# Kernel optimization log

Measured on AMD Instinct MI355X. Metric: run time of the kernel, lower is better.

## Reference

```python
import jax, jax.numpy as jnp
import numpy as np

B, H, W, C = 4, 64, 64, 64
DK = C // 8  # key/query channels from Conv2D(filters=channels//8)


def setup_inputs() -> dict:
    key = jax.random.key(0)
    ks = jax.random.split(key, 4)
    x = jax.random.normal(ks[0], (B, H, W, C), dtype=jnp.float32)
    # he_normal-ish scale for 1x1 conv kernels (fan_in = C)
    s = np.sqrt(2.0 / C).astype(np.float32)
    Wf = jax.random.normal(ks[1], (C, DK), dtype=jnp.float32) * s
    Wg = jax.random.normal(ks[2], (C, DK), dtype=jnp.float32) * s
    Wh = jax.random.normal(ks[3], (C, C), dtype=jnp.float32) * s
    bf = jnp.zeros((DK,), dtype=jnp.float32)
    bg = jnp.zeros((DK,), dtype=jnp.float32)
    bh = jnp.zeros((C,), dtype=jnp.float32)
    return {"x": x, "Wf": Wf, "bf": bf, "Wg": Wg, "bg": bg, "Wh": Wh, "bh": bh}


def reference(x, Wf, bf, Wg, bg, Wh, bh):
    b, h, w, c = x.shape
    n = h * w
    xf = x.reshape(b, n, c)  # 1x1 conv == per-position linear over flattened spatial dims
    f = xf @ Wf + bf         # [B, N, DK]
    g = xf @ Wg + bg         # [B, N, DK]
    v = xf @ Wh + bh         # [B, N, C]
    # attention = softmax(g @ f^T) over keys (tf.nn.softmax default: last axis)
    scores = jnp.einsum('bnd,bmd->bnm', g, f)   # [B, N, N]
    attn = jax.nn.softmax(scores, axis=-1)
    out = jnp.einsum('bnm,bmc->bnc', attn, v)   # [B, N, C]
    return out
```

## Files before the change

### kernel.cpp

```cpp
#include <hip/hip_runtime.h>
#include <hip/hip_bf16.h>
#include <hip/hip_fp16.h>

typedef _Float16 half8_t  __attribute__((ext_vector_type(8)));
typedef short    short8_t __attribute__((ext_vector_type(8)));
typedef short    short4_t __attribute__((ext_vector_type(4)));
typedef float    f32x4    __attribute__((ext_vector_type(4)));

#define LOG2E 1.44269504088896f

__device__ __forceinline__ unsigned pack_bf16_2(float lo, float hi) {
  float2 f2; f2.x = lo; f2.y = hi;
  __hip_bfloat162 h2 = __float22bfloat162_rn(f2);
  return *reinterpret_cast<unsigned*>(&h2);
}

__global__ __launch_bounds__(512) void prep_kernel(
    const float* __restrict__ x,
    const float* __restrict__ Wf, const float* __restrict__ bf,
    const float* __restrict__ Wg, const float* __restrict__ bg,
    const float* __restrict__ Wh, const float* __restrict__ bh,
    _Float16* __restrict__ fh, _Float16* __restrict__ gh,
    unsigned short* __restrict__ vT)
{
  __shared__ _Float16 WtT[80 * 72];
  __shared__ float ball[80];
  const int t = threadIdx.x;

  {
    int c = t >> 3, d = t & 7;
    WtT[d * 72 + c]       = (_Float16)Wf[t];
    WtT[(8 + d) * 72 + c] = (_Float16)(Wg[t] * LOG2E);
  }
#pragma unroll
  for (int rep = 0; rep < 2; rep++) {
    int i4 = t + rep * 512;
    float4 wv4 = *(const float4*)(Wh + i4 * 4);
    int c  = i4 >> 4;
    int ch = (i4 & 15) * 4;
    WtT[(16 + ch + 0) * 72 + c] = (_Float16)wv4.x;
    WtT[(16 + ch + 1) * 72 + c] = (_Float16)wv4.y;
    WtT[(16 + ch + 2) * 72 + c] = (_Float16)wv4.z;
    WtT[(16 + ch + 3) * 72 + c] = (_Float16)wv4.w;
  }
  if (t < 80) ball[t] = (t < 8) ? bf[t] : (t < 16) ? bg[t - 8] * LOG2E : bh[t - 16];
  __syncthreads();

  const int lane = t & 63, wv = t >> 6;
  const int quad = lane >> 4, l15 = lane & 15;
  const int wr   = wv & 3;
  const int hsel = wv >> 2;
  const int p0  = blockIdx.x * 64;
  const int row = p0 + wr * 16 + l15;

  const float* xr = x + (size_t)row * 64 + quad * 8;
  float4 xa = *(const float4*)(xr);
  float4 xb = *(const float4*)(xr + 4);
  float4 xc = *(const float4*)(xr + 32);
  float4 xd = *(const float4*)(xr + 36);
  half8_t a0, a1;
  a0[0]=(_Float16)xa.x; a0[1]=(_Float16)xa.y; a0[2]=(_Float16)xa.z; a0[3]=(_Float16)xa.w;
  a0[4]=(_Float16)xb.x; a0[5]=(_Float16)xb.y; a0[6]=(_Float16)xb.z; a0[7]=(_Float16)xb.w;
  a1[0]=(_Float16)xc.x; a1[1]=(_Float16)xc.y; a1[2]=(_Float16)xc.z; a1[3]=(_Float16)xc.w;
  a1[4]=(_Float16)xd.x; a1[5]=(_Float16)xd.y; a1[6]=(_Float16)xd.z; a1[7]=(_Float16)xd.w;

  const f32x4 zc = {0.f, 0.f, 0.f, 0.f};
  const int b     = p0 >> 12;
  const int nbase = (p0 & 4095) + wr * 16 + quad * 4;
  const int kblock = nbase >> 5;
  const int r0     = nbase & 31;
  const int q8 = r0 >> 3, j8 = r0 & 7;
  const int slot0 = (j8 < 4) ? (q8 * 4 + j8) : (16 + q8 * 4 + (j8 - 4));
  const size_t fbase_out = ((size_t)b * 4096 + (kblock << 5) + slot0) * 8;
  const size_t gbase_out = ((size_t)p0 + wr * 16 + quad * 4) * 8;
  const size_t vbase_out = (((size_t)b * 128 + kblock) << 11) + r0;

  if (hsel == 0) {
    {
      const _Float16* wt = &WtT[l15 * 72 + quad * 8];
      half8_t b0 = *(const half8_t*)(wt);
      half8_t b1 = *(const half8_t*)(wt + 32);
      f32x4 d = __builtin_amdgcn_mfma_f32_16x16x32_f16(a0, b0, zc, 0, 0, 0);
      d = __builtin_amdgcn_mfma_f32_16x16x32_f16(a1, b1, d, 0, 0, 0);
      const float bias = ball[l15];
      if (l15 < 8) {
#pragma unroll
        for (int reg = 0; reg < 4; reg++)
          fh[fbase_out + (size_t)reg * 8 + l15] = (_Float16)(d[reg] + bias);
      } else {
#pragma unroll
        for (int reg = 0; reg < 4; reg++)
          gh[gbase_out + (size_t)reg * 8 + (l15 - 8)] = (_Float16)(d[reg] + bias);
      }
    }
#pragma unroll
    for (int nt = 1; nt < 3; nt++) {
      const int ch0 = nt * 16 + l15;
      const _Float16* wt = &WtT[ch0 * 72 + quad * 8];
      half8_t b0 = *(const half8_t*)(wt);
      half8_t b1 = *(const half8_t*)(wt + 32);
      f32x4 d = __builtin_amdgcn_mfma_f32_16x16x32_f16(a0, b0, zc, 0, 0, 0);
      d = __builtin_amdgcn_mfma_f32_16x16x32_f16(a1, b1, d, 0, 0, 0);
      const float bias = ball[ch0];
      const int vch = ch0 - 16;
      union { unsigned u[2]; short4_t s; } pk;
      pk.u[0] = pack_bf16_2(d[0] + bias, d[1] + bias);
      pk.u[1] = pack_bf16_2(d[2] + bias, d[3] + bias);
      *(short4_t*)(vT + vbase_out + (size_t)vch * 32) = pk.s;
    }
  } else {
#pragma unroll
    for (int nt = 3; nt < 5; nt++) {
      const int ch0 = nt * 16 + l15;
      const _Float16* wt = &WtT[ch0 * 72 + quad * 8];
      half8_t b0 = *(const half8_t*)(wt);
      half8_t b1 = *(const half8_t*)(wt + 32);
      f32x4 d = __builtin_amdgcn_mfma_f32_16x16x32_f16(a0, b0, zc, 0, 0, 0);
      d = __builtin_amdgcn_mfma_f32_16x16x32_f16(a1, b1, d, 0, 0, 0);
      const float bias = ball[ch0];
      const int vch = ch0 - 16;
      union { unsigned u[2]; short4_t s; } pk;
      pk.u[0] = pack_bf16_2(d[0] + bias, d[1] + bias);
      pk.u[1] = pack_bf16_2(d[2] + bias, d[3] + bias);
      *(short4_t*)(vT + vbase_out + (size_t)vch * 32) = pk.s;
    }
  }
}

__device__ __forceinline__ void compute_chunk(
    const half8_t& f0, const half8_t& f1,
    const short8_t& v0, const short8_t& v1,
    const short8_t& v2, const short8_t& v3,
    const half8_t (&gfrag)[4], const short8_t& ones8,
    f32x4 (&acc)[4][4], f32x4 (&acc4)[4])
{
  const f32x4 zc = {0.f, 0.f, 0.f, 0.f};
  __builtin_amdgcn_s_setprio(1);
#pragma unroll
  for (int tt = 0; tt < 4; tt++) {
    f32x4 s0 = __builtin_amdgcn_mfma_f32_16x16x32_f16(f0, gfrag[tt], zc, 0, 0, 0);
    f32x4 s1 = __builtin_amdgcn_mfma_f32_16x16x32_f16(f1, gfrag[tt], zc, 0, 0, 0);
    float p00 = __builtin_amdgcn_exp2f(s0[0]), p01 = __builtin_amdgcn_exp2f(s0[1]);
    float p02 = __builtin_amdgcn_exp2f(s0[2]), p03 = __builtin_amdgcn_exp2f(s0[3]);
    float p10 = __builtin_amdgcn_exp2f(s1[0]), p11 = __builtin_amdgcn_exp2f(s1[1]);
    float p12 = __builtin_amdgcn_exp2f(s1[2]), p13 = __builtin_amdgcn_exp2f(s1[3]);
    union { unsigned u[4]; short8_t v; } pu;
    pu.u[0] = pack_bf16_2(p00, p01);
    pu.u[1] = pack_bf16_2(p02, p03);
    pu.u[2] = pack_bf16_2(p10, p11);
    pu.u[3] = pack_bf16_2(p12, p13);
    short8_t pfrag = pu.v;
    acc[tt][0] = __builtin_amdgcn_mfma_f32_16x16x32_bf16(v0, pfrag, acc[tt][0], 0, 0, 0);
    acc[tt][1] = __builtin_amdgcn_mfma_f32_16x16x32_bf16(v1, pfrag, acc[tt][1], 0, 0, 0);
    acc[tt][2] = __builtin_amdgcn_mfma_f32_16x16x32_bf16(v2, pfrag, acc[tt][2], 0, 0, 0);
    acc[tt][3] = __builtin_amdgcn_mfma_f32_16x16x32_bf16(v3, pfrag, acc[tt][3], 0, 0, 0);
    acc4[tt]   = __builtin_amdgcn_mfma_f32_16x16x32_bf16(ones8, pfrag, acc4[tt], 0, 0, 0);
  }
  __builtin_amdgcn_s_setprio(0);
}

__global__ __launch_bounds__(512, 2) void attn_kernel(
    const _Float16* __restrict__ fh,
    const _Float16* __restrict__ gh,
    const unsigned short* __restrict__ vT,
    float* __restrict__ out)
{
  const int N    = 4096;
  const int lane = threadIdx.x & 63;
  const int w    = threadIdx.x >> 6;
  const int quad = lane >> 4;
  const int l15  = lane & 15;

  __shared__ float red[7][64][17];

  const int xcd = blockIdx.x & 7;
  const int b   = xcd >> 1;
  const int qg  = ((blockIdx.x >> 3) << 1) + (xcd & 1);
  const int q0  = qg * 64;
  const int kbase = w * 512;
  const int rot = ((qg >> 1) & 15) + ((w >> 2) << 3);

  const _Float16* fbase = fh + (size_t)b * N * 8;
  const _Float16* gbase = gh + (size_t)b * N * 8;
  const short*    vbat  = (const short*)vT + (size_t)b * 262144 + (l15 << 5) + (quad << 3);

  half8_t gfrag[4] = {{}, {}, {}, {}};
  if (quad == 0) {
#pragma unroll
    for (int tt = 0; tt < 4; tt++)
      gfrag[tt] = *(const half8_t*)(gbase + (size_t)(q0 + tt * 16 + l15) * 8);
  }

  const f32x4 zc = {0.f, 0.f, 0.f, 0.f};
  f32x4 acc[4][4];
  f32x4 acc4[4];
#pragma unroll
  for (int tt = 0; tt < 4; tt++) {
    acc4[tt] = zc;
#pragma unroll
    for (int ct = 0; ct < 4; ct++) acc[tt][ct] = zc;
  }

  short8_t ones8;
#pragma unroll
  for (int i = 0; i < 8; i++) ones8[i] = (short)0x3F80;

#define KOFF(j) (kbase + ((((j) + rot) & 15) << 5))
#define LOADC(k, F0, F1, V0, V1, V2, V3)                                  \
  {                                                                       \
    const int kk = (k);                                                   \
    if (quad == 0) {                                                      \
      F0 = *(const half8_t*)(fbase + (size_t)(kk + l15) * 8);             \
      F1 = *(const half8_t*)(fbase + (size_t)(kk + 16 + l15) * 8);        \
    }                                                                     \
    const short* vk = vbat + ((size_t)(kk >> 5) << 11);                   \
    V0 = *(const short8_t*)(vk);                                          \
    V1 = *(const short8_t*)(vk + 512);                                    \
    V2 = *(const short8_t*)(vk + 1024);                                   \
    V3 = *(const short8_t*)(vk + 1536);                                   \
  }

  half8_t  fA0 = {}, fA1 = {}, fB0 = {}, fB1 = {};
  half8_t  fC0 = {}, fC1 = {}, fD0 = {}, fD1 = {};
  short8_t vA0, vA1, vA2, vA3, vB0, vB1, vB2, vB3;
  short8_t vC0, vC1, vC2, vC3, vD0, vD1, vD2, vD3;

  LOADC(KOFF(0), fA0, fA1, vA0, vA1, vA2, vA3);
  LOADC(KOFF(1), fB0, fB1, vB0, vB1, vB2, vB3);

#pragma unroll 1
  for (int cc = 0; cc < 16; cc += 4) {
    LOADC(KOFF(cc + 2), fC0, fC1, vC0, vC1, vC2, vC3);
    LOADC(KOFF(cc + 3), fD0, fD1, vD0, vD1, vD2, vD3);
    __builtin_amdgcn_sched_barrier(0);
    compute_chunk(fA0, fA1, vA0, vA1, vA2, vA3, gfrag, ones8, acc, acc4);
    compute_chunk(fB0, fB1, vB0, vB1, vB2, vB3, gfrag, ones8, acc, acc4);
    if (cc + 4 < 16) {
      LOADC(KOFF(cc + 4), fA0, fA1, vA0, vA1, vA2, vA3);
      LOADC(KOFF(cc + 5), fB0, fB1, vB0, vB1, vB2, vB3);
      __builtin_amdgcn_sched_barrier(0);
    }
    compute_chunk(fC0, fC1, vC0, vC1, vC2, vC3, gfrag, ones8, acc, acc4);
    compute_chunk(fD0, fD1, vD0, vD1, vD2, vD3, gfrag, ones8, acc, acc4);
  }
#undef LOADC
#undef KOFF

#pragma unroll
  for (int tt = 0; tt < 4; tt++) {
    if (w > 0) {
      float* p = &red[w - 1][lane][0];
#pragma unroll
      for (int ct = 0; ct < 4; ct++)
#pragma unroll
        for (int reg = 0; reg < 4; reg++) p[ct * 4 + reg] = acc[tt][ct][reg];
      p[16] = acc4[tt][0];
    }
    __syncthreads();
    if (w == 0) {
#pragma unroll
      for (int ww = 0; ww < 7; ww++) {
        const float* p = &red[ww][lane][0];
#pragma unroll
        for (int reg = 0; reg < 4; reg++) {
          acc[tt][0][reg] += p[0 + reg];
          acc[tt][1][reg] += p[4 + reg];
          acc[tt][2][reg] += p[8 + reg];
          acc[tt][3][reg] += p[12 + reg];
        }
        acc4[tt][0] += p[16];
      }
    }
    if (tt < 3) __syncthreads();
  }

  if (w == 0) {
#pragma unroll
    for (int tt = 0; tt < 4; tt++) {
      const float inv = 1.0f / acc4[tt][0];
      float* ob = out + ((size_t)b * N + q0 + tt * 16 + l15) * 64 + (quad << 2);
      *(f32x4*)(ob)      = acc[tt][0] * inv;
      *(f32x4*)(ob + 16) = acc[tt][1] * inv;
      *(f32x4*)(ob + 32) = acc[tt][2] * inv;
      *(f32x4*)(ob + 48) = acc[tt][3] * inv;
    }
  }
}

extern "C" void kernel_launch(void* const* d_in, const int* in_sizes, int n_in,
                              void* d_out, int out_size, void* d_ws, size_t ws_size,
                              hipStream_t stream) {
  const float* x  = (const float*)d_in[0];
  const float* Wf = (const float*)d_in[1];
  const float* bf = (const float*)d_in[2];
  const float* Wg = (const float*)d_in[3];
  const float* bg = (const float*)d_in[4];
  const float* Wh = (const float*)d_in[5];
  const float* bh = (const float*)d_in[6];
  float* out = (float*)d_out;

  char* ws = (char*)d_ws;
  _Float16* fh = (_Float16*)ws;
  _Float16* gh = (_Float16*)(ws + 262144);
  unsigned short* vT = (unsigned short*)(ws + 524288);

  prep_kernel<<<256, 512, 0, stream>>>(x, Wf, bf, Wg, bg, Wh, bh, fh, gh, vT);
  attn_kernel<<<256, 512, 0, stream>>>(fh, gh, vT, out);
}
```

Measured before the change: 89.33 us.

## Halve queries per block, double grid and raise occupancy with lighter prefetch

Each attention block now handles 32 queries instead of 64, so the grid doubles to 512 blocks and launch bounds request 4 blocks per CU. The software pipeline shrinks from four register-buffered chunks to two, and f loads are decoupled from V loads, which lowers register pressure. This aims to improve latency hiding through occupancy, not deep prefetch. The cost is that K/V tiles are re-read twice as often per query, and each block's cross-wave LDS reduction is amortized over fewer queries.

Result: slower. 93.11 us (+4.2%).

```diff
diff --git a/kernel.cpp b/kernel.cpp
--- a/kernel.cpp
+++ b/kernel.cpp
@@ -131,13 +131,13 @@
     const half8_t& f0, const half8_t& f1,
     const short8_t& v0, const short8_t& v1,
     const short8_t& v2, const short8_t& v3,
-    const half8_t (&gfrag)[4], const short8_t& ones8,
-    f32x4 (&acc)[4][4], f32x4 (&acc4)[4])
+    const half8_t (&gfrag)[2], const short8_t& ones8,
+    f32x4 (&acc)[2][4], f32x4 (&acc4)[2])
 {
   const f32x4 zc = {0.f, 0.f, 0.f, 0.f};
   __builtin_amdgcn_s_setprio(1);
 #pragma unroll
-  for (int tt = 0; tt < 4; tt++) {
+  for (int tt = 0; tt < 2; tt++) {
     f32x4 s0 = __builtin_amdgcn_mfma_f32_16x16x32_f16(f0, gfrag[tt], zc, 0, 0, 0);
     f32x4 s1 = __builtin_amdgcn_mfma_f32_16x16x32_f16(f1, gfrag[tt], zc, 0, 0, 0);
     float p00 = __builtin_amdgcn_exp2f(s0[0]), p01 = __builtin_amdgcn_exp2f(s0[1]);
@@ -159,7 +159,7 @@
   __builtin_amdgcn_s_setprio(0);
 }
 
-__global__ __launch_bounds__(512, 2) void attn_kernel(
+__global__ __launch_bounds__(512, 4) void attn_kernel(
     const _Float16* __restrict__ fh,
     const _Float16* __restrict__ gh,
     const unsigned short* __restrict__ vT,
@@ -176,7 +176,7 @@
   const int xcd = blockIdx.x & 7;
   const int b   = xcd >> 1;
   const int qg  = ((blockIdx.x >> 3) << 1) + (xcd & 1);
-  const int q0  = qg * 64;
+  const int q0  = qg * 32;
   const int kbase = w * 512;
   const int rot = ((qg >> 1) & 15) + ((w >> 2) << 3);
 
@@ -184,18 +184,18 @@
   const _Float16* gbase = gh + (size_t)b * N * 8;
   const short*    vbat  = (const short*)vT + (size_t)b * 262144 + (l15 << 5) + (quad << 3);
 
-  half8_t gfrag[4] = {{}, {}, {}, {}};
+  half8_t gfrag[2] = {{}, {}};
   if (quad == 0) {
 #pragma unroll
-    for (int tt = 0; tt < 4; tt++)
+    for (int tt = 0; tt < 2; tt++)
       gfrag[tt] = *(const half8_t*)(gbase + (size_t)(q0 + tt * 16 + l15) * 8);
   }
 
   const f32x4 zc = {0.f, 0.f, 0.f, 0.f};
-  f32x4 acc[4][4];
-  f32x4 acc4[4];
-#pragma unroll
-  for (int tt = 0; tt < 4; tt++) {
+  f32x4 acc[2][4];
+  f32x4 acc4[2];
+#pragma unroll
+  for (int tt = 0; tt < 2; tt++) {
     acc4[tt] = zc;
 #pragma unroll
     for (int ct = 0; ct < 4; ct++) acc[tt][ct] = zc;
@@ -206,48 +206,42 @@
   for (int i = 0; i < 8; i++) ones8[i] = (short)0x3F80;
 
 #define KOFF(j) (kbase + ((((j) + rot) & 15) << 5))
-#define LOADC(k, F0, F1, V0, V1, V2, V3)                                  \
+#define LOADV(k, V0, V1, V2, V3)                                          \
   {                                                                       \
-    const int kk = (k);                                                   \
-    if (quad == 0) {                                                      \
-      F0 = *(const half8_t*)(fbase + (size_t)(kk + l15) * 8);             \
-      F1 = *(const half8_t*)(fbase + (size_t)(kk + 16 + l15) * 8);        \
-    }                                                                     \
-    const short* vk = vbat + ((size_t)(kk >> 5) << 11);                   \
+    const short* vk = vbat + ((size_t)((k) >> 5) << 11);                  \
     V0 = *(const short8_t*)(vk);                                          \
     V1 = *(const short8_t*)(vk + 512);                                    \
     V2 = *(const short8_t*)(vk + 1024);                                   \
     V3 = *(const short8_t*)(vk + 1536);                                   \
   }
-
-  half8_t  fA0 = {}, fA1 = {}, fB0 = {}, fB1 = {};
-  half8_t  fC0 = {}, fC1 = {}, fD0 = {}, fD1 = {};
-  short8_t vA0, vA1, vA2, vA3, vB0, vB1, vB2, vB3;
-  short8_t vC0, vC1, vC2, vC3, vD0, vD1, vD2, vD3;
-
-  LOADC(KOFF(0), fA0, fA1, vA0, vA1, vA2, vA3);
-  LOADC(KOFF(1), fB0, fB1, vB0, vB1, vB2, vB3);
+#define LOADF(k, F0, F1)                                                  \
+  if (quad == 0) {                                                        \
+    F0 = *(const half8_t*)(fbase + (size_t)((k) + l15) * 8);              \
+    F1 = *(const half8_t*)(fbase + (size_t)((k) + 16 + l15) * 8);         \
+  }
+
+  half8_t  fa0 = {}, fa1 = {};
+  short8_t va0, va1, va2, va3, vb0, vb1, vb2, vb3;
+
+  LOADV(KOFF(0), va0, va1, va2, va3);
 
 #pragma unroll 1
-  for (int cc = 0; cc < 16; cc += 4) {
-    LOADC(KOFF(cc + 2), fC0, fC1, vC0, vC1, vC2, vC3);
-    LOADC(KOFF(cc + 3), fD0, fD1, vD0, vD1, vD2, vD3);
-    __builtin_amdgcn_sched_barrier(0);
-    compute_chunk(fA0, fA1, vA0, vA1, vA2, vA3, gfrag, ones8, acc, acc4);
-    compute_chunk(fB0, fB1, vB0, vB1, vB2, vB3, gfrag, ones8, acc, acc4);
-    if (cc + 4 < 16) {
-      LOADC(KOFF(cc + 4), fA0, fA1, vA0, vA1, vA2, vA3);
-      LOADC(KOFF(cc + 5), fB0, fB1, vB0, vB1, vB2, vB3);
-      __builtin_amdgcn_sched_barrier(0);
-    }
-    compute_chunk(fC0, fC1, vC0, vC1, vC2, vC3, gfrag, ones8, acc, acc4);
-    compute_chunk(fD0, fD1, vD0, vD1, vD2, vD3, gfrag, ones8, acc, acc4);
-  }
-#undef LOADC
+  for (int cc = 0; cc < 16; cc += 2) {
+    LOADV(KOFF(cc + 1), vb0, vb1, vb2, vb3);
+    LOADF(KOFF(cc), fa0, fa1);
+    compute_chunk(fa0, fa1, va0, va1, va2, va3, gfrag, ones8, acc, acc4);
+    if (cc + 2 < 16) {
+      LOADV(KOFF(cc + 2), va0, va1, va2, va3);
+    }
+    LOADF(KOFF(cc + 1), fa0, fa1);
+    compute_chunk(fa0, fa1, vb0, vb1, vb2, vb3, gfrag, ones8, acc, acc4);
+  }
+#undef LOADV
+#undef LOADF
 #undef KOFF
 
 #pragma unroll
-  for (int tt = 0; tt < 4; tt++) {
+  for (int tt = 0; tt < 2; tt++) {
     if (w > 0) {
       float* p = &red[w - 1][lane][0];
 #pragma unroll
@@ -271,12 +265,12 @@
         acc4[tt][0] += p[16];
       }
     }
-    if (tt < 3) __syncthreads();
+    if (tt < 1) __syncthreads();
   }
 
   if (w == 0) {
 #pragma unroll
-    for (int tt = 0; tt < 4; tt++) {
+    for (int tt = 0; tt < 2; tt++) {
       const float inv = 1.0f / acc4[tt][0];
       float* ob = out + ((size_t)b * N + q0 + tt * 16 + l15) * 64 + (quad << 2);
       *(f32x4*)(ob)      = acc[tt][0] * inv;
@@ -305,5 +299,5 @@
   unsigned short* vT = (unsigned short*)(ws + 524288);
 
   prep_kernel<<<256, 512, 0, stream>>>(x, Wf, bf, Wg, bg, Wh, bh, fh, gh, vT);
-  attn_kernel<<<256, 512, 0, stream>>>(fh, gh, vT, out);
-}
+  attn_kernel<<<512, 512, 0, stream>>>(fh, gh, vT, out);
+}
```
